# Kernel optimization log

Hardware: AMD Instinct MI355X
Metric: run time of the kernel (lower is better)

The kernel has to match this reference:

```python
import jax, jax.numpy as jnp
import numpy as np

B, S, D, H = 2, 2048, 1024, 16
DK = D // H

def setup_inputs() -> dict:
    key = jax.random.key(0)
    ks = jax.random.split(key, 5)
    std = 1.0 / np.sqrt(D)
    return {
        "x": jax.random.normal(ks[0], (B, S, D), dtype=jnp.float32),
        "wq": jax.random.normal(ks[1], (D, D), dtype=jnp.float32) * std,
        "wk": jax.random.normal(ks[2], (D, D), dtype=jnp.float32) * std,
        "wv": jax.random.normal(ks[3], (D, D), dtype=jnp.float32) * std,
        "wo": jax.random.normal(ks[4], (D, D), dtype=jnp.float32) * std,
    }

def reference(x, wq, wk, wv, wo):
    b, s, d = x.shape
    # torch Linear(bias=False): x @ W.T
    q = (x @ wq.T).reshape(b, s, H, DK).transpose(0, 2, 1, 3)  # [b,h,s,dk]
    k = (x @ wk.T).reshape(b, s, H, DK).transpose(0, 2, 1, 3)
    v = (x @ wv.T).reshape(b, s, H, DK).transpose(0, 2, 1, 3)
    scale = jnp.sqrt(jnp.asarray(DK, dtype=x.dtype))
    scores = jnp.einsum('bhqd,bhkd->bhqk', q, k) / scale  # [b,h,s,s]
    # causal mask (masking=True): lower-triangular kept, rest -inf
    causal = jnp.tril(jnp.ones((s, s), dtype=bool))
    scores = jnp.where(causal[None, None], scores, -jnp.inf)
    attn = jax.nn.softmax(scores, axis=-1)
    out = jnp.einsum('bhqk,bhkd->bhqd', attn, v)  # [b,h,s,dk]
    out = out.transpose(0, 2, 1, 3).reshape(b, s, d)
    return out @ wo.T
```

## Files before the change

### kernel.cpp

```cpp
#include <hip/hip_runtime.h>

#define LB __launch_bounds__(256)

typedef __bf16 bf16x8 __attribute__((ext_vector_type(8)));
typedef float f32x4 __attribute__((ext_vector_type(4)));
typedef float f32x16 __attribute__((ext_vector_type(16)));
typedef unsigned int u32;
typedef unsigned int u32x2 __attribute__((ext_vector_type(2)));

constexpr int B = 2, S = 2048, D = 1024, H = 16, DK = 64;
constexpr int M = B * S;
constexpr int K = D;

__device__ __forceinline__ unsigned short f2bf(float f) {
    union { float f; unsigned u; } v; v.f = f;
    unsigned r = v.u + 0x7fffu + ((v.u >> 16) & 1u);
    return (unsigned short)(r >> 16);
}

__device__ __forceinline__ u32 pk2bf(float lo, float hi) {
    union { __bf16 h[2]; u32 w; } u;
    u.h[0] = (__bf16)lo; u.h[1] = (__bf16)hi;
    return u.w;
}

__device__ __forceinline__ float bf2f(unsigned short h) {
    union { unsigned u; float f; } v; v.u = ((unsigned)h) << 16;
    return v.f;
}

__device__ __forceinline__ void gld_lds16(const unsigned short* g, unsigned short* l) {
    __builtin_amdgcn_global_load_lds(
        (const __attribute__((address_space(1))) unsigned int*)g,
        (__attribute__((address_space(3))) unsigned int*)l, 16, 0, 0);
}

__global__ LB void cvt_all(const float* __restrict__ x,  const float* __restrict__ wq,
                           const float* __restrict__ wk, const float* __restrict__ wv,
                           const float* __restrict__ wo, unsigned short* __restrict__ dst) {
    const size_t NX = (size_t)M * D;
    const size_t NW = (size_t)D * D;
    size_t i = ((size_t)blockIdx.x * 256 + threadIdx.x) * 4;
    if (i >= NX + 4 * NW) return;
    const float* src; size_t off;
    if      (i < NX)          { src = x;  off = i; }
    else if (i < NX + NW)     { src = wq; off = i - NX; }
    else if (i < NX + 2 * NW) { src = wk; off = i - NX - NW; }
    else if (i < NX + 3 * NW) { src = wv; off = i - NX - 2 * NW; }
    else                      { src = wo; off = i - NX - 3 * NW; }
    float4 f = *reinterpret_cast<const float4*>(src + off);
    ushort4 o;
    o.x = f2bf(f.x); o.y = f2bf(f.y); o.z = f2bf(f.z); o.w = f2bf(f.w);
    *reinterpret_cast<ushort4*>(dst + i) = o;
}

__global__ LB void gemm_qkv(const unsigned short* __restrict__ A,
                            const unsigned short* __restrict__ wqb,
                            const unsigned short* __restrict__ wkb,
                            const unsigned short* __restrict__ wvb,
                            unsigned short* __restrict__ qo,
                            unsigned short* __restrict__ ko,
                            unsigned short* __restrict__ vo) {
    __shared__ __align__(16) unsigned short lA[128 * 32];
    __shared__ __align__(16) unsigned short lB[128 * 32];
    const int z = blockIdx.y;
    const unsigned short* W = (z == 0) ? wqb : ((z == 1) ? wkb : wvb);
    int bid = blockIdx.x;
    int m0 = (((bid >> 6) << 3) | (bid & 7)) * 128;
    int n0 = ((bid >> 3) & 7) * 128;
    int t = threadIdx.x;
    int w = t >> 6, lane = t & 63;
    int r = lane & 15, g = lane >> 4;
    int wr = w >> 1, wc = w & 1;
    int rowT = t >> 2, colOff = (t & 3) * 8;

    f32x4 acc[4][4];
#pragma unroll
    for (int mi = 0; mi < 4; ++mi)
#pragma unroll
        for (int ni = 0; ni < 4; ++ni) acc[mi][ni] = f32x4{0.f, 0.f, 0.f, 0.f};

    for (int k0 = 0; k0 < K; k0 += 32) {
        gld_lds16(A + (size_t)(m0 + rowT) * K + k0 + colOff,      lA + (w * 64) * 8);
        gld_lds16(A + (size_t)(m0 + 64 + rowT) * K + k0 + colOff, lA + (256 + w * 64) * 8);
        gld_lds16(W + (size_t)(n0 + rowT) * K + k0 + colOff,      lB + (w * 64) * 8);
        gld_lds16(W + (size_t)(n0 + 64 + rowT) * K + k0 + colOff, lB + (256 + w * 64) * 8);
        __syncthreads();
        bf16x8 af[4], bfr[4];
#pragma unroll
        for (int mi = 0; mi < 4; ++mi)
            af[mi] = *reinterpret_cast<const bf16x8*>(&lA[(wr * 64 + mi * 16 + r) * 32 + g * 8]);
#pragma unroll
        for (int ni = 0; ni < 4; ++ni)
            bfr[ni] = *reinterpret_cast<const bf16x8*>(&lB[(wc * 64 + ni * 16 + r) * 32 + g * 8]);
#pragma unroll
        for (int mi = 0; mi < 4; ++mi)
#pragma unroll
            for (int ni = 0; ni < 4; ++ni)
                acc[mi][ni] = __builtin_amdgcn_mfma_f32_16x16x32_bf16(af[mi], bfr[ni], acc[mi][ni], 0, 0, 0);
        __syncthreads();
    }

    const float QSCALE = 0.125f * 1.44269504088896341f;
    float scale = (z == 0) ? QSCALE : 1.0f;
    unsigned short* dst = (z == 0) ? qo : ((z == 1) ? ko : vo);
#pragma unroll
    for (int mi = 0; mi < 4; ++mi)
#pragma unroll
        for (int ni = 0; ni < 4; ++ni)
#pragma unroll
            for (int j = 0; j < 4; ++j) {
                int row = m0 + wr * 64 + mi * 16 + g * 4 + j;
                int col = n0 + wc * 64 + ni * 16 + r;
                int b = row >> 11, s = row & (S - 1);
                int h = col >> 6, dk = col & 63;
                size_t bh = (size_t)(b * H + h);
                unsigned short val = f2bf(acc[mi][ni][j] * scale);
                if (z == 0) {
                    dst[(bh * S + s) * DK + dk] = val;
                } else if (z == 1) {
                    int kt32 = s >> 5, q5k = s & 31;
                    int dsi = dk >> 4, hlk = (dk >> 3) & 1, e = dk & 7;
                    dst[(((bh * 64 + kt32) * 4 + dsi) * 64 + (hlk * 32 + q5k)) * 8 + e] = val;
                } else {
                    int ktile = s >> 6, ks2 = (s >> 4) & 3, hlv = (s >> 3) & 1, e = s & 7;
                    int rh = dk >> 5, q5r = dk & 31;
                    dst[(((bh * 32 + ktile) * 8 + rh * 4 + ks2) * 64 + (hlv * 32 + q5r)) * 8 + e] = val;
                }
            }
}

__global__ LB void out_gemm(const unsigned short* __restrict__ A,
                            const unsigned short* __restrict__ W,
                            float* __restrict__ out) {
    __shared__ __align__(16) unsigned short lA[128 * 32];
    __shared__ __align__(16) unsigned short lB[64 * 32];
    int bid = blockIdx.x;
    int m0 = (((bid >> 7) << 3) | (bid & 7)) * 128;
    int n0 = ((bid >> 3) & 15) * 64;
    int t = threadIdx.x;
    int w = t >> 6, lane = t & 63;
    int r = lane & 15, g = lane >> 4;
    int wr = w >> 1, wc = w & 1;
    int rowT = t >> 2, colOff = (t & 3) * 8;

    f32x4 acc[4][2];
#pragma unroll
    for (int mi = 0; mi < 4; ++mi)
#pragma unroll
        for (int ni = 0; ni < 2; ++ni) acc[mi][ni] = f32x4{0.f, 0.f, 0.f, 0.f};

    for (int k0 = 0; k0 < K; k0 += 32) {
        gld_lds16(A + (size_t)(m0 + rowT) * K + k0 + colOff,      lA + (w * 64) * 8);
        gld_lds16(A + (size_t)(m0 + 64 + rowT) * K + k0 + colOff, lA + (256 + w * 64) * 8);
        gld_lds16(W + (size_t)(n0 + rowT) * K + k0 + colOff,      lB + (w * 64) * 8);
        __syncthreads();
        bf16x8 af[4], bfr[2];
#pragma unroll
        for (int mi = 0; mi < 4; ++mi)
            af[mi] = *reinterpret_cast<const bf16x8*>(&lA[(wr * 64 + mi * 16 + r) * 32 + g * 8]);
#pragma unroll
        for (int ni = 0; ni < 2; ++ni)
            bfr[ni] = *reinterpret_cast<const bf16x8*>(&lB[(wc * 32 + ni * 16 + r) * 32 + g * 8]);
#pragma unroll
        for (int mi = 0; mi < 4; ++mi)
#pragma unroll
            for (int ni = 0; ni < 2; ++ni)
                acc[mi][ni] = __builtin_amdgcn_mfma_f32_16x16x32_bf16(af[mi], bfr[ni], acc[mi][ni], 0, 0, 0);
        __syncthreads();
    }

#pragma unroll
    for (int mi = 0; mi < 4; ++mi)
#pragma unroll
        for (int ni = 0; ni < 2; ++ni)
#pragma unroll
            for (int j = 0; j < 4; ++j) {
                int row = m0 + wr * 64 + mi * 16 + g * 4 + j;
                int col = n0 + wc * 32 + ni * 16 + r;
                out[(size_t)row * D + col] = acc[mi][ni][j];
            }
}

__global__ __launch_bounds__(64) void flash_attn(
        const unsigned short* __restrict__ q,
        const unsigned short* __restrict__ kmat,
        const unsigned short* __restrict__ vt,
        unsigned short* __restrict__ p0,
        unsigned short* __restrict__ p1,
        float* __restrict__ l0,
        float* __restrict__ l1) {
    int bid = blockIdx.x;
    int qt = 63 - (bid >> 6);
    int half = (bid >> 5) & 1;
    int bh = bid & 31;
    int b = bh >> 4, hd = bh & 15;
    int q0 = qt << 5;
    int nt = (qt + 2) >> 1;
    int nh1 = (nt + 1) >> 1;
    int n_lo = half ? nh1 : 0;
    int n_hi = half ? nt : nh1;

    unsigned short* Pd = half ? p1 : p0;
    float* Ld = half ? l1 : l0;

    int l = threadIdx.x;
    int q5 = l & 31, hl = l >> 5;
    int qglob = q0 + q5;

    const unsigned short* qp = q    + (size_t)bh * S * DK;
    const unsigned short* kf = kmat + (size_t)bh * S * DK;
    const unsigned short* vf = vt   + (size_t)bh * S * DK;

    bf16x8 ones;
#pragma unroll
    for (int i = 0; i < 8; ++i) ones[i] = (__bf16)1.0f;

    const f32x16 z16 = {0,0,0,0,0,0,0,0,0,0,0,0,0,0,0,0};

    bf16x8 qf[4];
#pragma unroll
    for (int dsi = 0; dsi < 4; ++dsi)
        qf[dsi] = *reinterpret_cast<const bf16x8*>(qp + (size_t)qglob * DK + dsi * 16 + hl * 8);

    f32x16 acc0 = z16, acc1 = z16, accl = z16;

    auto loadK = [&](bf16x8 (&kr)[8], int kb) {
        const unsigned short* base = kf + (size_t)(kb >> 5) * 4 * 512 + l * 8;
#pragma unroll
        for (int dsi = 0; dsi < 4; ++dsi) {
            kr[dsi]     = *reinterpret_cast<const bf16x8*>(base + dsi * 512);
            kr[4 + dsi] = *reinterpret_cast<const bf16x8*>(base + (4 + dsi) * 512);
        }
    };
    auto loadV = [&](bf16x8 (&vr)[8], int kb) {
        const unsigned short* base = vf + (size_t)(kb >> 6) * 8 * 512 + l * 8;
#pragma unroll
        for (int i2 = 0; i2 < 8; ++i2)
            vr[i2] = *reinterpret_cast<const bf16x8*>(base + i2 * 512);
    };
    auto compute = [&](bf16x8 (&kr)[8], bf16x8 (&vr)[8], int kb) {
        f32x16 st0 = __builtin_amdgcn_mfma_f32_32x32x16_bf16(kr[0], qf[0], z16, 0, 0, 0);
        f32x16 st1 = __builtin_amdgcn_mfma_f32_32x32x16_bf16(kr[4], qf[0], z16, 0, 0, 0);
#pragma unroll
        for (int dsi = 1; dsi < 4; ++dsi) {
            st0 = __builtin_amdgcn_mfma_f32_32x32x16_bf16(kr[dsi],     qf[dsi], st0, 0, 0, 0);
            st1 = __builtin_amdgcn_mfma_f32_32x32x16_bf16(kr[4 + dsi], qf[dsi], st1, 0, 0, 0);
        }
        if (kb + 31 > q0) {
#pragma unroll
            for (int r = 0; r < 16; ++r) {
                int kv = kb + (r & 3) + 8 * (r >> 2) + 4 * hl;
                st0[r] = (kv <= qglob) ? st0[r] : -1e30f;
            }
        }
        if (kb + 63 > q0) {
#pragma unroll
            for (int r = 0; r < 16; ++r) {
                int kv = kb + 32 + (r & 3) + 8 * (r >> 2) + 4 * hl;
                st1[r] = (kv <= qglob) ? st1[r] : -1e30f;
            }
        }
#pragma unroll
        for (int r = 0; r < 16; ++r) { st0[r] = exp2f(st0[r]); st1[r] = exp2f(st1[r]); }
        u32 pk[2][8];
#pragma unroll
        for (int rg = 0; rg < 4; ++rg) {
            pk[0][2*rg]   = pk2bf(st0[4*rg],   st0[4*rg+1]);
            pk[0][2*rg+1] = pk2bf(st0[4*rg+2], st0[4*rg+3]);
            pk[1][2*rg]   = pk2bf(st1[4*rg],   st1[4*rg+1]);
            pk[1][2*rg+1] = pk2bf(st1[4*rg+2], st1[4*rg+3]);
        }
        union PF { bf16x8 vv; u32 w[4]; } pf[4];
#pragma unroll
        for (int ti2 = 0; ti2 < 2; ++ti2)
#pragma unroll
            for (int s = 0; s < 2; ++s) {
                u32x2 r0 = __builtin_amdgcn_permlane32_swap(pk[ti2][4*s],   pk[ti2][4*s+2], false, false);
                u32x2 r1 = __builtin_amdgcn_permlane32_swap(pk[ti2][4*s+1], pk[ti2][4*s+3], false, false);
                PF f;
                f.w[0] = r0[0]; f.w[1] = r1[0];
                f.w[2] = r0[1]; f.w[3] = r1[1];
                pf[ti2*2+s] = f;
            }
#pragma unroll
        for (int ks = 0; ks < 4; ++ks) {
            acc0 = __builtin_amdgcn_mfma_f32_32x32x16_bf16(vr[ks],     pf[ks].vv, acc0, 0, 0, 0);
            acc1 = __builtin_amdgcn_mfma_f32_32x32x16_bf16(vr[4 + ks], pf[ks].vv, acc1, 0, 0, 0);
            accl = __builtin_amdgcn_mfma_f32_32x32x16_bf16(ones,       pf[ks].vv, accl, 0, 0, 0);
        }
    };

    bf16x8 ka[8], kb2[8], va[8], vb2[8];
    int it = n_lo;
    if (it < n_hi) {
        loadK(ka, it << 6);
        loadV(va, it << 6);
        while (true) {
            if (it + 1 < n_hi) { loadK(kb2, (it + 1) << 6); loadV(vb2, (it + 1) << 6); }
            compute(ka, va, it << 6);
            ++it; if (it >= n_hi) break;
            if (it + 1 < n_hi) { loadK(ka, (it + 1) << 6); loadV(va, (it + 1) << 6); }
            compute(kb2, vb2, it << 6);
            ++it; if (it >= n_hi) break;
        }
    }

    if (hl == 0) Ld[(size_t)bh * S + q0 + q5] = accl[0];
    size_t obase = ((size_t)(b * S + qglob)) * D + hd * DK;
#pragma unroll
    for (int rg = 0; rg < 4; ++rg) {
        uint2 wd;
        wd.x = pk2bf(acc0[4*rg],   acc0[4*rg+1]);
        wd.y = pk2bf(acc0[4*rg+2], acc0[4*rg+3]);
        *reinterpret_cast<uint2*>(Pd + obase + rg * 8 + hl * 4) = wd;
        uint2 we;
        we.x = pk2bf(acc1[4*rg],   acc1[4*rg+1]);
        we.y = pk2bf(acc1[4*rg+2], acc1[4*rg+3]);
        *reinterpret_cast<uint2*>(Pd + obase + 32 + rg * 8 + hl * 4) = we;
    }
}

__global__ LB void merge_o(unsigned short* __restrict__ p0,
                           const unsigned short* __restrict__ p1,
                           const float* __restrict__ l0,
                           const float* __restrict__ l1) {
    size_t i = ((size_t)blockIdx.x * 256 + threadIdx.x) * 8;
    int row = (int)(i >> 10);
    int col = (int)(i & 1023);
    int h = col >> 6;
    int b = row >> 11, s = row & (S - 1);
    size_t bh = (size_t)(b * H + h);
    float inv = 1.0f / (l0[bh * S + s] + l1[bh * S + s]);
    ushort4 a0 = *reinterpret_cast<const ushort4*>(p0 + i);
    ushort4 a1 = *reinterpret_cast<const ushort4*>(p0 + i + 4);
    ushort4 b0 = *reinterpret_cast<const ushort4*>(p1 + i);
    ushort4 b1 = *reinterpret_cast<const ushort4*>(p1 + i + 4);
    ushort4 o0, o1;
    o0.x = f2bf((bf2f(a0.x) + bf2f(b0.x)) * inv);
    o0.y = f2bf((bf2f(a0.y) + bf2f(b0.y)) * inv);
    o0.z = f2bf((bf2f(a0.z) + bf2f(b0.z)) * inv);
    o0.w = f2bf((bf2f(a0.w) + bf2f(b0.w)) * inv);
    o1.x = f2bf((bf2f(a1.x) + bf2f(b1.x)) * inv);
    o1.y = f2bf((bf2f(a1.y) + bf2f(b1.y)) * inv);
    o1.z = f2bf((bf2f(a1.z) + bf2f(b1.z)) * inv);
    o1.w = f2bf((bf2f(a1.w) + bf2f(b1.w)) * inv);
    *reinterpret_cast<ushort4*>(p0 + i)     = o0;
    *reinterpret_cast<ushort4*>(p0 + i + 4) = o1;
}

extern "C" void kernel_launch(void* const* d_in, const int* in_sizes, int n_in,
                              void* d_out, int out_size, void* d_ws, size_t ws_size,
                              hipStream_t stream) {
    const float* x  = (const float*)d_in[0];
    const float* wq = (const float*)d_in[1];
    const float* wk = (const float*)d_in[2];
    const float* wv = (const float*)d_in[3];
    const float* wo = (const float*)d_in[4];
    char* ws = (char*)d_ws;
    unsigned short* xb  = (unsigned short*)(ws);
    unsigned short* wqb = (unsigned short*)(ws + (size_t)(8  << 20));
    unsigned short* wkb = (unsigned short*)(ws + (size_t)(10 << 20));
    unsigned short* wvb = (unsigned short*)(ws + (size_t)(12 << 20));
    unsigned short* wob = (unsigned short*)(ws + (size_t)(14 << 20));
    unsigned short* qb  = (unsigned short*)(ws + (size_t)(16 << 20));
    unsigned short* kb  = (unsigned short*)(ws + (size_t)(24 << 20));
    unsigned short* vtb = (unsigned short*)(ws + (size_t)(32 << 20));
    unsigned short* p0  = (unsigned short*)(ws + (size_t)(40 << 20));
    unsigned short* p1  = (unsigned short*)(ws);
    float* l0 = (float*)(ws + (size_t)(8 << 20));
    float* l1 = (float*)(ws + (size_t)(9 << 20));

    cvt_all<<<8192, 256, 0, stream>>>(x, wq, wk, wv, wo, xb);

    gemm_qkv<<<dim3(256, 3), 256, 0, stream>>>(xb, wqb, wkb, wvb, qb, kb, vtb);
    flash_attn<<<4096, 64, 0, stream>>>(qb, kb, vtb, p0, p1, l0, l1);
    merge_o<<<2048, 256, 0, stream>>>(p0, p1, l0, l1);
    out_gemm<<<512, 256, 0, stream>>>(p0, wob, (float*)d_out);
}
```

Before: 120.1 us.

## Drop register double-buffering in flash attention, raise occupancy, use raw v_exp

Replaces the ping-pong register prefetch of K/V tiles with a simple per-iteration loop that loads K, runs QK MFMAs, then loads V before the softmax. It sets a min-blocks hint of 4 in launch bounds so more waves can be resident, and swaps exp2f for an inline v_exp_f32 to skip the range-handling code. The intent is to trade explicit in-wave prefetch for latency hiding across waves. The risk is exposed load latency if occupancy does not rise enough, and denormal or edge handling differences in exp.

Result: no change. 120.8 us (+0.6%).

```diff
diff --git a/kernel.cpp b/kernel.cpp
--- a/kernel.cpp
+++ b/kernel.cpp
@@ -27,6 +27,12 @@
 __device__ __forceinline__ float bf2f(unsigned short h) {
     union { unsigned u; float f; } v; v.u = ((unsigned)h) << 16;
     return v.f;
+}
+
+__device__ __forceinline__ float fexp2(float x) {
+    float y;
+    asm("v_exp_f32 %0, %1" : "=v"(y) : "v"(x));
+    return y;
 }
 
 __device__ __forceinline__ void gld_lds16(const unsigned short* g, unsigned short* l) {
@@ -182,7 +188,7 @@
             }
 }
 
-__global__ __launch_bounds__(64) void flash_attn(
+__global__ __launch_bounds__(64, 4) void flash_attn(
         const unsigned short* __restrict__ q,
         const unsigned short* __restrict__ kmat,
         const unsigned short* __restrict__ vt,
@@ -225,21 +231,18 @@
 
     f32x16 acc0 = z16, acc1 = z16, accl = z16;
 
-    auto loadK = [&](bf16x8 (&kr)[8], int kb) {
-        const unsigned short* base = kf + (size_t)(kb >> 5) * 4 * 512 + l * 8;
-#pragma unroll
-        for (int dsi = 0; dsi < 4; ++dsi) {
-            kr[dsi]     = *reinterpret_cast<const bf16x8*>(base + dsi * 512);
-            kr[4 + dsi] = *reinterpret_cast<const bf16x8*>(base + (4 + dsi) * 512);
-        }
-    };
-    auto loadV = [&](bf16x8 (&vr)[8], int kb) {
-        const unsigned short* base = vf + (size_t)(kb >> 6) * 8 * 512 + l * 8;
-#pragma unroll
-        for (int i2 = 0; i2 < 8; ++i2)
-            vr[i2] = *reinterpret_cast<const bf16x8*>(base + i2 * 512);
-    };
-    auto compute = [&](bf16x8 (&kr)[8], bf16x8 (&vr)[8], int kb) {
+#pragma unroll 1
+    for (int it = n_lo; it < n_hi; ++it) {
+        int kb = it << 6;
+        bf16x8 kr[8];
+        {
+            const unsigned short* base = kf + (size_t)(kb >> 5) * 4 * 512 + l * 8;
+#pragma unroll
+            for (int dsi = 0; dsi < 4; ++dsi) {
+                kr[dsi]     = *reinterpret_cast<const bf16x8*>(base + dsi * 512);
+                kr[4 + dsi] = *reinterpret_cast<const bf16x8*>(base + (4 + dsi) * 512);
+            }
+        }
         f32x16 st0 = __builtin_amdgcn_mfma_f32_32x32x16_bf16(kr[0], qf[0], z16, 0, 0, 0);
         f32x16 st1 = __builtin_amdgcn_mfma_f32_32x32x16_bf16(kr[4], qf[0], z16, 0, 0, 0);
 #pragma unroll
@@ -247,6 +250,13 @@
             st0 = __builtin_amdgcn_mfma_f32_32x32x16_bf16(kr[dsi],     qf[dsi], st0, 0, 0, 0);
             st1 = __builtin_amdgcn_mfma_f32_32x32x16_bf16(kr[4 + dsi], qf[dsi], st1, 0, 0, 0);
         }
+        bf16x8 vr[8];
+        {
+            const unsigned short* base = vf + (size_t)(kb >> 6) * 8 * 512 + l * 8;
+#pragma unroll
+            for (int i2 = 0; i2 < 8; ++i2)
+                vr[i2] = *reinterpret_cast<const bf16x8*>(base + i2 * 512);
+        }
         if (kb + 31 > q0) {
 #pragma unroll
             for (int r = 0; r < 16; ++r) {
@@ -262,7 +272,7 @@
             }
         }
 #pragma unroll
-        for (int r = 0; r < 16; ++r) { st0[r] = exp2f(st0[r]); st1[r] = exp2f(st1[r]); }
+        for (int r = 0; r < 16; ++r) { st0[r] = fexp2(st0[r]); st1[r] = fexp2(st1[r]); }
         u32 pk[2][8];
 #pragma unroll
         for (int rg = 0; rg < 4; ++rg) {
@@ -288,21 +298,6 @@
             acc0 = __builtin_amdgcn_mfma_f32_32x32x16_bf16(vr[ks],     pf[ks].vv, acc0, 0, 0, 0);
             acc1 = __builtin_amdgcn_mfma_f32_32x32x16_bf16(vr[4 + ks], pf[ks].vv, acc1, 0, 0, 0);
             accl = __builtin_amdgcn_mfma_f32_32x32x16_bf16(ones,       pf[ks].vv, accl, 0, 0, 0);
-        }
-    };
-
-    bf16x8 ka[8], kb2[8], va[8], vb2[8];
-    int it = n_lo;
-    if (it < n_hi) {
-        loadK(ka, it << 6);
-        loadV(va, it << 6);
-        while (true) {
-            if (it + 1 < n_hi) { loadK(kb2, (it + 1) << 6); loadV(vb2, (it + 1) << 6); }
-            compute(ka, va, it << 6);
-            ++it; if (it >= n_hi) break;
-            if (it + 1 < n_hi) { loadK(ka, (it + 1) << 6); loadV(va, (it + 1) << 6); }
-            compute(kb2, vb2, it << 6);
-            ++it; if (it >= n_hi) break;
         }
     }
 
```
